# Kernel tuning notes

Measured on AMD Instinct MI355X. Metric: run time of the kernel, lower is better.

Reference implementation:

```python
import jax, jax.numpy as jnp
import numpy as np

B, I, O, N = 65536, 256, 32, 8


def chebyshev_basis(x, n):
    """Chebyshev polynomials T_0..T_{n-1} of x. x: [B, I] -> [B, I, n]."""
    T = [jnp.ones_like(x), x]
    for _ in range(n - 2):
        T.append(2.0 * x * T[-1] - T[-2])
    return jnp.stack(T[:n], axis=-1)


def setup_inputs() -> dict:
    key = jax.random.key(0)
    k1, k2 = jax.random.split(key)
    # inputs live on [-1, 1], the natural Chebyshev domain
    x = jax.random.uniform(k1, (B, I), jnp.float32, minval=-1.0, maxval=1.0)
    # weight init mirrors torch: uniform(-weight_magnitude/in, weight_magnitude/in)
    w = jax.random.uniform(k2, (O, I, N), jnp.float32, minval=-1.0 / I, maxval=1.0 / I)
    return {"x": x, "w": w}


def reference(x, w):
    n = w.shape[-1]
    phi = chebyshev_basis(x, n)          # [B, I, n] basis expansion
    out = jnp.einsum("bin,oin->bo", phi, w)  # weighted contraction
    return out
```

## Files before the change

### kernel.cpp

```cpp
#include <hip/hip_runtime.h>
#include <hip/hip_bf16.h>


typedef __attribute__((ext_vector_type(8)))  short bf16x8;
typedef __attribute__((ext_vector_type(16))) float f32x16;
typedef __attribute__((ext_vector_type(4)))  float f32x4;

__device__ __forceinline__ short f2b(float f) {
    __hip_bfloat16 h = __float2bfloat16(f);
    short s;
    __builtin_memcpy(&s, &h, sizeof(s));
    return s;
}

__device__ __forceinline__ unsigned pkbf(float lo, float hi) {
    __hip_bfloat162 h2 = __float22bfloat162_rn(make_float2(lo, hi));
    unsigned u;
    __builtin_memcpy(&u, &h2, 4);
    return u;
}

__global__ __launch_bounds__(256) void prep_w_kernel(const float* __restrict__ w,
                                                     short* __restrict__ wB) {
    int idx = blockIdx.x * 256 + threadIdx.x;
    int kc2 = idx >> 9;
    int l   = (idx >> 3) & 63;
    int jj  = idx & 7;
    int o = l & 31, g = l >> 5;
    int i = 2 * kc2 + (jj >> 2);
    int n = 4 * g + (jj & 3);
    wB[idx] = f2b(w[(o * 256 + i) * 8 + n]);
}

__global__ __launch_bounds__(256, 5) void cheb_mm_kernel(const float* __restrict__ x,
                                                         const short* __restrict__ wB,
                                                         float* __restrict__ out) {
    __shared__ float smem[8192];
    const int tid = threadIdx.x;
    const int wv  = tid >> 6;
    const int l   = tid & 63;
    const int g   = l >> 5;
    const int r0  = l & 31;
    const long long rowB = (long long)blockIdx.x * 32;

    {
        const float4* xg4 = (const float4*)(x + rowB * 256);
        float4 stg[8];
        #pragma unroll
        for (int q = 0; q < 8; ++q)
            stg[q] = xg4[q * 256 + tid];
        float2* s2 = (float2*)smem;
        #pragma unroll
        for (int q = 0; q < 8; ++q) {
            int slot = q * 256 + tid;
            int row = slot >> 6, f4 = slot & 63;
            int p0 = 2 * f4, p1 = 2 * f4 + 1;
            int d0 = (p0 & ~31) + ((p0 & 31) ^ (row & 31));
            int d1 = (p1 & ~31) + ((p1 & 31) ^ (row & 31));
            s2[row * 128 + d0] = make_float2(stg[q].x, stg[q].y);
            s2[row * 128 + d1] = make_float2(stg[q].z, stg[q].w);
        }
    }
    __syncthreads();

    f32x16 accA{}, accB{};
    const bf16x8* wq = (const bf16x8*)wB + wv * 2048 + l;
    const float* sf = smem;
    const int xbase = r0 * 256 + wv * 64 + g;

#if __has_builtin(__builtin_amdgcn_permlane32_swap)
    bf16x8 bfc[4];
    float  xc[2];
    #pragma unroll
    for (int p = 0; p < 4; ++p) bfc[p] = wq[p * 64];
    xc[0] = sf[xbase + ((0 ^ r0) << 1)];
    xc[1] = sf[xbase + ((1 ^ r0) << 1)];

    #pragma unroll
    for (int t = 0; t < 32; ++t) {
        const bf16x8 bfrag = bfc[t & 3];
        const float  xv    = xc[t & 1];
        if (t + 4 < 32) bfc[t & 3] = wq[(t + 4) * 64];
        if (t + 2 < 32) xc[t & 1] = sf[xbase + (((t + 2) ^ r0) << 1)];

        const float x2 = xv + xv;
        const float T2 = fmaf(x2, xv, -1.f);
        const float T3 = fmaf(x2, T2, -xv);
        const float T4 = fmaf(x2, T3, -T2);
        const float T5 = fmaf(x2, T4, -T3);
        const float T6 = fmaf(x2, T5, -T4);
        const float T7 = fmaf(x2, T6, -T5);
        unsigned R0 = pkbf(1.f, xv);
        unsigned R1 = pkbf(T2, T3);
        unsigned R2 = pkbf(T4, T5);
        unsigned R3 = pkbf(T6, T7);
        auto r02 = __builtin_amdgcn_permlane32_swap(R0, R2, false, false);
        auto r13 = __builtin_amdgcn_permlane32_swap(R1, R3, false, false);
        union { unsigned u[4]; bf16x8 v; } af;
        af.u[0] = r02[0]; af.u[1] = r13[0];
        af.u[2] = r02[1]; af.u[3] = r13[1];
        if (t & 1)
            accB = __builtin_amdgcn_mfma_f32_32x32x16_bf16(af.v, bfrag, accB, 0, 0, 0);
        else
            accA = __builtin_amdgcn_mfma_f32_32x32x16_bf16(af.v, bfrag, accA, 0, 0, 0);
    }
#else
    const float2* srow = (const float2*)smem + r0 * 128 + wv * 32;
    #pragma unroll 8
    for (int t = 0; t < 32; ++t) {
        const bf16x8 bfrag = wq[t * 64];
        const float2 xv = srow[t ^ r0];
        const float xa = xv.x, xb = xv.y;
        const float x2a = xa + xa, x2b = xb + xb;
        const float a2 = x2a * xa - 1.f;
        const float a3 = x2a * a2 - xa;
        const float a4 = x2a * a3 - a2;
        const float a5 = x2a * a4 - a3;
        const float b2 = x2b * xb - 1.f;
        const float b3 = x2b * b2 - xb;
        const float b4 = x2b * b3 - b2;
        const float b5 = x2b * b4 - b3;
        const float ua0 = g ? a4 : 1.f;
        const float ua1 = g ? a5 : xa;
        const float ua2 = x2a * ua1 - ua0;
        const float ua3 = x2a * ua2 - ua1;
        const float ub0 = g ? b4 : 1.f;
        const float ub1 = g ? b5 : xb;
        const float ub2 = x2b * ub1 - ub0;
        const float ub3 = x2b * ub2 - ub1;
        bf16x8 afrag;
        afrag[0] = f2b(ua0); afrag[1] = f2b(ua1);
        afrag[2] = f2b(ua2); afrag[3] = f2b(ua3);
        afrag[4] = f2b(ub0); afrag[5] = f2b(ub1);
        afrag[6] = f2b(ub2); afrag[7] = f2b(ub3);
        if (t & 1)
            accB = __builtin_amdgcn_mfma_f32_32x32x16_bf16(afrag, bfrag, accB, 0, 0, 0);
        else
            accA = __builtin_amdgcn_mfma_f32_32x32x16_bf16(afrag, bfrag, accA, 0, 0, 0);
    }
#endif
    const f32x16 acc = accA + accB;

    __syncthreads();
    #pragma unroll
    for (int r = 0; r < 16; ++r) {
        const int rloc = (r & 3) + 8 * (r >> 2) + 4 * g;
        smem[wv * 1024 + rloc * 32 + r0] = acc[r];
    }
    __syncthreads();

    {
        float* op = out + rowB * 32;
        const int f = tid * 4;
        f32x4 v0 = *(const f32x4*)&smem[f];
        f32x4 v1 = *(const f32x4*)&smem[1024 + f];
        f32x4 v2 = *(const f32x4*)&smem[2048 + f];
        f32x4 v3 = *(const f32x4*)&smem[3072 + f];
        f32x4 s = (v0 + v1) + (v2 + v3);
        *(f32x4*)(op + f) = s;
    }
}

extern "C" void kernel_launch(void* const* d_in, const int* in_sizes, int n_in,
                              void* d_out, int out_size, void* d_ws, size_t ws_size,
                              hipStream_t stream) {
    const float* x = (const float*)d_in[0];
    const float* w = (const float*)d_in[1];
    float* out = (float*)d_out;
    short* wB = (short*)d_ws;

    prep_w_kernel<<<256, 256, 0, stream>>>(w, wB);
    cheb_mm_kernel<<<2048, 256, 0, stream>>>(x, wB, out);
}
```

Before: 32.24 us.

## Make x staging wave-private to drop block barriers and prefetch weights early

Each wave now loads only its own 64-column K-slice of x into shared memory, with the XOR swizzle recomputed for that layout. Since no wave reads another wave's x data, the barrier after staging is removed. The epilogue writes partial sums into the wave's own slice, so the barrier before those writes is also gone. The first weight fragments are loaded before x staging so their latency overlaps the x loads, and the non-permlane fallback path is deleted. The price is a less linear global load pattern (256-byte row segments per wave instead of fully contiguous block reads) and dependence on the permlane32_swap builtin being available.

```diff
diff --git a/kernel.cpp b/kernel.cpp
--- a/kernel.cpp
+++ b/kernel.cpp
@@ -43,36 +43,35 @@
     const int r0  = l & 31;
     const long long rowB = (long long)blockIdx.x * 32;
 
+    const bf16x8* wq = (const bf16x8*)wB + wv * 2048 + l;
+    bf16x8 bfc[4];
+    #pragma unroll
+    for (int p = 0; p < 4; ++p) bfc[p] = wq[p * 64];
+
     {
         const float4* xg4 = (const float4*)(x + rowB * 256);
+        const int f4l = l & 15;
+        const int rsub = l >> 4;
         float4 stg[8];
         #pragma unroll
         for (int q = 0; q < 8; ++q)
-            stg[q] = xg4[q * 256 + tid];
-        float2* s2 = (float2*)smem;
+            stg[q] = xg4[(q * 4 + rsub) * 64 + wv * 16 + f4l];
         #pragma unroll
         for (int q = 0; q < 8; ++q) {
-            int slot = q * 256 + tid;
-            int row = slot >> 6, f4 = slot & 63;
-            int p0 = 2 * f4, p1 = 2 * f4 + 1;
-            int d0 = (p0 & ~31) + ((p0 & 31) ^ (row & 31));
-            int d1 = (p1 & ~31) + ((p1 & 31) ^ (row & 31));
-            s2[row * 128 + d0] = make_float2(stg[q].x, stg[q].y);
-            s2[row * 128 + d1] = make_float2(stg[q].z, stg[q].w);
+            const int row  = q * 4 + rsub;
+            const int base = row * 256 + wv * 64;
+            const int s    = row & 31;
+            const int p0 = 2 * f4l, p1 = 2 * f4l + 1;
+            *(float2*)&smem[base + 2 * (p0 ^ s)] = make_float2(stg[q].x, stg[q].y);
+            *(float2*)&smem[base + 2 * (p1 ^ s)] = make_float2(stg[q].z, stg[q].w);
         }
     }
-    __syncthreads();
 
     f32x16 accA{}, accB{};
-    const bf16x8* wq = (const bf16x8*)wB + wv * 2048 + l;
     const float* sf = smem;
     const int xbase = r0 * 256 + wv * 64 + g;
 
-#if __has_builtin(__builtin_amdgcn_permlane32_swap)
-    bf16x8 bfc[4];
-    float  xc[2];
-    #pragma unroll
-    for (int p = 0; p < 4; ++p) bfc[p] = wq[p * 64];
+    float xc[2];
     xc[0] = sf[xbase + ((0 ^ r0) << 1)];
     xc[1] = sf[xbase + ((1 ^ r0) << 1)];
 
@@ -104,58 +103,25 @@
         else
             accA = __builtin_amdgcn_mfma_f32_32x32x16_bf16(af.v, bfrag, accA, 0, 0, 0);
     }
-#else
-    const float2* srow = (const float2*)smem + r0 * 128 + wv * 32;
-    #pragma unroll 8
-    for (int t = 0; t < 32; ++t) {
-        const bf16x8 bfrag = wq[t * 64];
-        const float2 xv = srow[t ^ r0];
-        const float xa = xv.x, xb = xv.y;
-        const float x2a = xa + xa, x2b = xb + xb;
-        const float a2 = x2a * xa - 1.f;
-        const float a3 = x2a * a2 - xa;
-        const float a4 = x2a * a3 - a2;
-        const float a5 = x2a * a4 - a3;
-        const float b2 = x2b * xb - 1.f;
-        const float b3 = x2b * b2 - xb;
-        const float b4 = x2b * b3 - b2;
-        const float b5 = x2b * b4 - b3;
-        const float ua0 = g ? a4 : 1.f;
-        const float ua1 = g ? a5 : xa;
-        const float ua2 = x2a * ua1 - ua0;
-        const float ua3 = x2a * ua2 - ua1;
-        const float ub0 = g ? b4 : 1.f;
-        const float ub1 = g ? b5 : xb;
-        const float ub2 = x2b * ub1 - ub0;
-        const float ub3 = x2b * ub2 - ub1;
-        bf16x8 afrag;
-        afrag[0] = f2b(ua0); afrag[1] = f2b(ua1);
-        afrag[2] = f2b(ua2); afrag[3] = f2b(ua3);
-        afrag[4] = f2b(ub0); afrag[5] = f2b(ub1);
-        afrag[6] = f2b(ub2); afrag[7] = f2b(ub3);
-        if (t & 1)
-            accB = __builtin_amdgcn_mfma_f32_32x32x16_bf16(afrag, bfrag, accB, 0, 0, 0);
-        else
-            accA = __builtin_amdgcn_mfma_f32_32x32x16_bf16(afrag, bfrag, accA, 0, 0, 0);
-    }
-#endif
     const f32x16 acc = accA + accB;
 
-    __syncthreads();
     #pragma unroll
     for (int r = 0; r < 16; ++r) {
         const int rloc = (r & 3) + 8 * (r >> 2) + 4 * g;
-        smem[wv * 1024 + rloc * 32 + r0] = acc[r];
+        smem[rloc * 256 + wv * 64 + r0] = acc[r];
     }
     __syncthreads();
 
     {
         float* op = out + rowB * 32;
-        const int f = tid * 4;
-        f32x4 v0 = *(const f32x4*)&smem[f];
-        f32x4 v1 = *(const f32x4*)&smem[1024 + f];
-        f32x4 v2 = *(const f32x4*)&smem[2048 + f];
-        f32x4 v3 = *(const f32x4*)&smem[3072 + f];
+        const int f   = tid * 4;
+        const int row = f >> 5;
+        const int c   = f & 31;
+        const int b   = row * 256 + c;
+        f32x4 v0 = *(const f32x4*)&smem[b];
+        f32x4 v1 = *(const f32x4*)&smem[b + 64];
+        f32x4 v2 = *(const f32x4*)&smem[b + 128];
+        f32x4 v3 = *(const f32x4*)&smem[b + 192];
         f32x4 s = (v0 + v1) + (v2 + v3);
         *(f32x4*)(op + f) = s;
     }
```

Result: faster. 31.05 us (-3.7%).
